# Kernel optimization log

Hardware: AMD Instinct MI355X
Metric: run time of the kernel (lower is better)

Reference implementation:

```python
import jax, jax.numpy as jnp
import numpy as np

B, T, M, D, L = 8, 4096, 32768, 128, 3  # L = ebm_GNN_layer_num - 1


def _lin(x, W, b):
    return x @ W + b


def setup_inputs() -> dict:
    key = jax.random.key(0)
    ks = jax.random.split(key, 24)
    s = 0.05
    inp = {
        "x_1st": jax.random.normal(ks[0], (B, T, 2, D), dtype=jnp.float32),
        "x_2nd": jax.random.normal(ks[1], (B, M, 4, D), dtype=jnp.float32),
        "A_causal": jax.random.uniform(ks[2], (B, 1, M), dtype=jnp.float32),
        "edge": jax.random.randint(ks[3], (2, M), 0, T, dtype=jnp.int64),
        # per-layer node/edge weights (stacked over L layers)
        "node_W": jax.random.normal(ks[4], (L, D, D)) * s,
        "node_b": jnp.zeros((L, D)),
        "mlp_W": jax.random.normal(ks[5], (L, D, D)) * s,
        "mlp_b": jnp.zeros((L, D)),
        "edgeL_W": jax.random.normal(ks[6], (L, D, D)) * s,
        "edgeL_b": jnp.zeros((L, D)),
        # node readout MLP: D -> 2D -> D -> 1
        "nro_W1": jax.random.normal(ks[7], (D, 2 * D)) * s, "nro_b1": jnp.zeros((2 * D,)),
        "nro_W2": jax.random.normal(ks[8], (2 * D, D)) * s, "nro_b2": jnp.zeros((D,)),
        "nro_W3": jax.random.normal(ks[9], (D, 1)) * s, "nro_b3": jnp.zeros((1,)),
        # edge readout MLP
        "ero_W1": jax.random.normal(ks[10], (D, 2 * D)) * s, "ero_b1": jnp.zeros((2 * D,)),
        "ero_W2": jax.random.normal(ks[11], (2 * D, D)) * s, "ero_b2": jnp.zeros((D,)),
        "ero_W3": jax.random.normal(ks[12], (D, 1)) * s, "ero_b3": jnp.zeros((1,)),
    }
    return inp


def reference(x_1st, x_2nd, A_causal, node_W, node_b, mlp_W, mlp_b,
              edgeL_W, edgeL_b, nro_W1, nro_b1, nro_W2, nro_b2, nro_W3, nro_b3,
              ero_W1, ero_b1, ero_W2, ero_b2, ero_W3, ero_b3, edge):
    ni = jnp.array([0, 0, 1, 1])  # node_i_indice
    nj = jnp.array([0, 1, 0, 1])  # node_j_indice
    e0, e1 = edge[0], edge[1]
    a = A_causal[:, 0, :, None, None]  # (B, M, 1, 1)
    xn, xe = x_1st, x_2nd
    for i in range(L):
        # --- node layer: gather -> mask-multiply -> scatter_add -> linear ---
        msg = xn[:, e1] * a                          # (B, M, 2, D)
        upd = jnp.zeros_like(xn).at[:, e0].add(msg)  # (B, T, 2, D)
        xn_new = _lin(xn + upd, node_W[i], node_b[i])
        # --- edge layer (uses updated node features, as in torch forward) ---
        ei = xn_new[:, e0][:, :, ni]                 # (B, M, 4, D)
        ej = xn_new[:, e1][:, :, nj]                 # (B, M, 4, D)
        xe_new = _lin(xe + _lin(ei + ej, mlp_W[i], mlp_b[i]), edgeL_W[i], edgeL_b[i])
        if i < L - 1:
            xn_new = jax.nn.relu(xn_new)
            xe_new = jax.nn.relu(xe_new)
        xn, xe = xn_new, xe_new
    # readouts (dropout=0, concat=False)
    h_node = _lin(jax.nn.relu(_lin(jax.nn.relu(_lin(xn, nro_W1, nro_b1)), nro_W2, nro_b2)), nro_W3, nro_b3)[..., 0]
    h_edge = _lin(jax.nn.relu(_lin(jax.nn.relu(_lin(xe, ero_W1, ero_b1)), ero_W2, ero_b2)), ero_W3, ero_b3)[..., 0]
    return h_node, h_edge  # (B,T,2), (B,M,4)
```

## Files before the change

### kernel.cpp

```cpp
#include <hip/hip_runtime.h>

#define NB 8
#define NT 4096
#define NM 32768
#define ND 128

typedef __attribute__((ext_vector_type(8))) short bf16x8;
typedef __attribute__((ext_vector_type(4))) float f32x4;
typedef __attribute__((ext_vector_type(4))) unsigned int u32x4;

#define MFMA(a,b,c) __builtin_amdgcn_mfma_f32_16x16x32_bf16(a,b,c,0,0,0)

__device__ __forceinline__ unsigned short f2bf(float x) {
  unsigned u = __float_as_uint(x);
  u += 0x7FFFu + ((u >> 16) & 1u);
  return (unsigned short)(u >> 16);
}
__device__ __forceinline__ float bf2f(unsigned short h) {
  return __uint_as_float(((unsigned)h) << 16);
}

__device__ __forceinline__ bf16x8 ldsFrag(const char* lds, int row, int kByte, int rowStride) {
  return *(const bf16x8*)(lds + ((row * rowStride + kByte) ^ ((row & 7) << 4)));
}

__global__ __launch_bounds__(256) void k_prep(
    const float* __restrict__ W, char* __restrict__ dst,
    int K, int N, int khShift, int perShift, int total)
{
  int i = blockIdx.x * 256 + threadIdx.x;
  if (i >= total) return;
  int m  = i >> perShift;
  int j  = i & ((1 << perShift) - 1);
  int n  = j >> khShift;
  int kh = j & ((1 << khShift) - 1);
  int k0 = kh << 3;
  const float* Wm = W + (size_t)m * K * N;
  char* dm = dst + (size_t)m * K * N * 2;
  unsigned short tmp[8];
  #pragma unroll
  for (int jj = 0; jj < 8; ++jj) tmp[jj] = f2bf(Wm[(k0 + jj) * N + n]);
  *(u32x4*)(dm + ((n * K * 2 + k0 * 2) ^ ((n & 7) << 4))) = *(u32x4*)tmp;
}

__global__ __launch_bounds__(256) void k_csr_count(const int* __restrict__ edge, int* deg) {
  int m = blockIdx.x * 256 + threadIdx.x;
  if (m < NM) atomicAdd(&deg[edge[m]], 1);
}
__global__ __launch_bounds__(64) void k_csr_scan(const int* __restrict__ deg,
                                                 int* __restrict__ off, int* __restrict__ cursor) {
  __shared__ int partial[64];
  int t = threadIdx.x;
  int base = t * 64;
  int sum = 0;
  for (int i = 0; i < 64; ++i) sum += deg[base + i];
  partial[t] = sum;
  __syncthreads();
  if (t == 0) {
    int run = 0;
    for (int i = 0; i < 64; ++i) { int v = partial[i]; partial[i] = run; run += v; }
  }
  __syncthreads();
  int run = partial[t];
  for (int i = 0; i < 64; ++i) {
    off[base + i] = run; cursor[base + i] = run;
    run += deg[base + i];
  }
  if (t == 63) off[NT] = NM;
}
__global__ __launch_bounds__(256) void k_csr_fill(const int* __restrict__ edge,
                                                  int* cursor, int* __restrict__ csr) {
  int m = blockIdx.x * 256 + threadIdx.x;
  if (m < NM) { int pos = atomicAdd(&cursor[edge[m]], 1); csr[pos] = m; }
}
__global__ __launch_bounds__(256) void k_csr_sort(const int* __restrict__ off, int* __restrict__ csr) {
  int n = blockIdx.x * 256 + threadIdx.x;
  if (n < NT) {
    int s = off[n], e = off[n + 1];
    for (int i = s + 1; i < e; ++i) {
      int v = csr[i]; int j = i - 1;
      while (j >= s && csr[j] > v) { csr[j + 1] = csr[j]; --j; }
      csr[j + 1] = v;
    }
  }
}

__global__ __launch_bounds__(256, 4) void k_node(
    const float* __restrict__ xnIn, float* __restrict__ xnOut,
    const float* __restrict__ A, const int* __restrict__ edge,
    const int* __restrict__ off, const int* __restrict__ csr,
    const char* __restrict__ WImg, const float* __restrict__ bias,
    int doReluIn, int nTiles)
{
  __shared__ __align__(16) char WT[128 * 256];
  __shared__ __align__(16) char xs[32 * 256];
  const int t = threadIdx.x;
  {
    const u32x4* s = (const u32x4*)WImg;
    u32x4* d = (u32x4*)WT;
    for (int i = t; i < 2048; i += 256) d[i] = s[i];
  }
  const int w   = t >> 6;
  const int l   = t & 63;
  const int l15 = l & 15;
  const int lg  = l >> 4;
  float bv2[2];
  #pragma unroll
  for (int fc = 0; fc < 2; ++fc) bv2[fc] = bias[w * 32 + fc * 16 + l15];
  const int gr = t >> 3;
  const int c0 = (t & 7) << 4;
  __syncthreads();

  for (int tile = blockIdx.x; tile < nTiles; tile += gridDim.x) {
    const int rowBase = tile << 5;
    {
      const int grow = rowBase + gr;
      const int ch   = grow & 1;
      const int node = (grow >> 1) & (NT - 1);
      const int b    = grow >> 13;
      f32x4 acc[4];
      {
        const float4* xr = (const float4*)(xnIn + (size_t)grow * ND + c0);
        #pragma unroll
        for (int q = 0; q < 4; ++q) {
          float4 v = xr[q];
          if (doReluIn) {
            v.x = fmaxf(v.x, 0.f); v.y = fmaxf(v.y, 0.f);
            v.z = fmaxf(v.z, 0.f); v.w = fmaxf(v.w, 0.f);
          }
          acc[q] = (f32x4){v.x, v.y, v.z, v.w};
        }
      }
      const int s = off[node], e = off[node + 1];
      for (int p = s; p < e; ++p) {
        int m = csr[p];
        float a = A[b * NM + m];
        int e1 = edge[NM + m];
        const float4* src = (const float4*)(xnIn + (size_t)(((b * NT + e1) << 1) + ch) * ND + c0);
        #pragma unroll
        for (int q = 0; q < 4; ++q) {
          float4 v = src[q];
          if (doReluIn) {
            v.x = fmaxf(v.x, 0.f); v.y = fmaxf(v.y, 0.f);
            v.z = fmaxf(v.z, 0.f); v.w = fmaxf(v.w, 0.f);
          }
          acc[q][0] = fmaf(a, v.x, acc[q][0]);
          acc[q][1] = fmaf(a, v.y, acc[q][1]);
          acc[q][2] = fmaf(a, v.z, acc[q][2]);
          acc[q][3] = fmaf(a, v.w, acc[q][3]);
        }
      }
      unsigned short tmp[8];
      #pragma unroll
      for (int q = 0; q < 2; ++q)
        #pragma unroll
        for (int j = 0; j < 4; ++j) tmp[q * 4 + j] = f2bf(acc[q][j]);
      *(u32x4*)(xs + ((gr * 256 + c0 * 2) ^ ((gr & 7) << 4))) = *(u32x4*)tmp;
      #pragma unroll
      for (int q = 0; q < 2; ++q)
        #pragma unroll
        for (int j = 0; j < 4; ++j) tmp[q * 4 + j] = f2bf(acc[2 + q][j]);
      *(u32x4*)(xs + ((gr * 256 + c0 * 2 + 16) ^ ((gr & 7) << 4))) = *(u32x4*)tmp;
    }
    __syncthreads();
    f32x4 acc2[2][2];
    #pragma unroll
    for (int fr = 0; fr < 2; ++fr)
      #pragma unroll
      for (int fc = 0; fc < 2; ++fc) acc2[fr][fc] = (f32x4){0.f, 0.f, 0.f, 0.f};
    #pragma unroll
    for (int ks = 0; ks < 4; ++ks) {
      int kb = ks * 64 + lg * 16;
      bf16x8 b0 = ldsFrag(WT, w * 32 + l15,      kb, 256);
      bf16x8 b1 = ldsFrag(WT, w * 32 + 16 + l15, kb, 256);
      bf16x8 a0 = ldsFrag(xs, l15,      kb, 256);
      bf16x8 a1 = ldsFrag(xs, 16 + l15, kb, 256);
      acc2[0][0] = MFMA(a0, b0, acc2[0][0]);
      acc2[0][1] = MFMA(a0, b1, acc2[0][1]);
      acc2[1][0] = MFMA(a1, b0, acc2[1][0]);
      acc2[1][1] = MFMA(a1, b1, acc2[1][1]);
    }
    __syncthreads();
    #pragma unroll
    for (int fr = 0; fr < 2; ++fr)
      #pragma unroll
      for (int fc = 0; fc < 2; ++fc) {
        int col = w * 32 + fc * 16 + l15;
        #pragma unroll
        for (int i = 0; i < 4; ++i) {
          int r = fr * 16 + lg * 4 + i;
          xnOut[(size_t)(rowBase + r) * ND + col] = acc2[fr][fc][i] + bv2[fc];
        }
      }
  }
}

template<int IN_F32>
__global__ __launch_bounds__(512, 4) void k_edge_mfma(
    const float* __restrict__ xn,
    const float* __restrict__ xeInF, const unsigned short* __restrict__ xeInH,
    unsigned short* xeOut,
    const int* __restrict__ edge,
    const char* __restrict__ WmImg, const float* __restrict__ bm,
    const char* __restrict__ WeImg, const float* __restrict__ be,
    int doReluOut, int nTiles)
{
  __shared__ __align__(16) char WmT[128 * 256];
  __shared__ __align__(16) char WeT[128 * 256];
  __shared__ __align__(16) char sA[64 * 256];
  const int t = threadIdx.x;
  {
    const u32x4* sm = (const u32x4*)WmImg;
    const u32x4* se = (const u32x4*)WeImg;
    u32x4* dm = (u32x4*)WmT;
    u32x4* de = (u32x4*)WeT;
    for (int i = t; i < 2048; i += 512) { dm[i] = sm[i]; de[i] = se[i]; }
  }
  const int w   = t >> 6;
  const int l   = t & 63;
  const int l15 = l & 15;
  const int lg  = l >> 4;
  const int rg2 = w >> 2;
  const int wc  = w & 3;
  float bmv[2], bev[2];
  #pragma unroll
  for (int fc = 0; fc < 2; ++fc) {
    int col = wc * 32 + fc * 16 + l15;
    bmv[fc] = bm[col];
    bev[fc] = be[col];
  }
  const int srow = t >> 3;
  __syncthreads();

  for (int tile = blockIdx.x; tile < nTiles; tile += gridDim.x) {
    const int rowBase = tile << 6;
    {
      int grow = rowBase + srow;
      int cch = grow & 3;
      int m = (grow >> 2) & (NM - 1);
      int b = grow >> 17;
      int e0 = edge[m], e1 = edge[NM + m];
      const float4* p0 = (const float4*)(xn + (size_t)((b * NT + e0) * 2 + (cch >> 1)) * ND);
      const float4* p1 = (const float4*)(xn + (size_t)((b * NT + e1) * 2 + (cch & 1)) * ND);
      #pragma unroll
      for (int hh = 0; hh < 2; ++hh) {
        int h = (t & 7) + hh * 8;
        float4 a0 = p0[h * 2], a1 = p0[h * 2 + 1];
        float4 c0 = p1[h * 2], c1 = p1[h * 2 + 1];
        unsigned short tmp[8];
        tmp[0] = f2bf(a0.x + c0.x); tmp[1] = f2bf(a0.y + c0.y);
        tmp[2] = f2bf(a0.z + c0.z); tmp[3] = f2bf(a0.w + c0.w);
        tmp[4] = f2bf(a1.x + c1.x); tmp[5] = f2bf(a1.y + c1.y);
        tmp[6] = f2bf(a1.z + c1.z); tmp[7] = f2bf(a1.w + c1.w);
        *(u32x4*)(sA + ((srow * 256 + h * 16) ^ ((srow & 7) << 4))) = *(u32x4*)tmp;
      }
    }
    float xev[2][2][4];
    #pragma unroll
    for (int fr = 0; fr < 2; ++fr)
      #pragma unroll
      for (int fc = 0; fc < 2; ++fc) {
        int col = wc * 32 + fc * 16 + l15;
        #pragma unroll
        for (int i = 0; i < 4; ++i) {
          int r = rg2 * 32 + fr * 16 + lg * 4 + i;
          size_t idx = (size_t)(rowBase + r) * ND + col;
          xev[fr][fc][i] = IN_F32 ? xeInF[idx] : bf2f(xeInH[idx]);
        }
      }
    __syncthreads();
    f32x4 acc[2][2];
    #pragma unroll
    for (int fr = 0; fr < 2; ++fr)
      #pragma unroll
      for (int fc = 0; fc < 2; ++fc) acc[fr][fc] = (f32x4){0.f, 0.f, 0.f, 0.f};
    #pragma unroll
    for (int ks = 0; ks < 4; ++ks) {
      int kb = ks * 64 + lg * 16;
      bf16x8 b0 = ldsFrag(WmT, wc * 32 + l15,      kb, 256);
      bf16x8 b1 = ldsFrag(WmT, wc * 32 + 16 + l15, kb, 256);
      #pragma unroll
      for (int fr = 0; fr < 2; ++fr) {
        bf16x8 a = ldsFrag(sA, rg2 * 32 + fr * 16 + l15, kb, 256);
        acc[fr][0] = MFMA(a, b0, acc[fr][0]);
        acc[fr][1] = MFMA(a, b1, acc[fr][1]);
      }
    }
    __syncthreads();
    #pragma unroll
    for (int fr = 0; fr < 2; ++fr)
      #pragma unroll
      for (int fc = 0; fc < 2; ++fc) {
        int col = wc * 32 + fc * 16 + l15;
        #pragma unroll
        for (int i = 0; i < 4; ++i) {
          int r = rg2 * 32 + fr * 16 + lg * 4 + i;
          float v = xev[fr][fc][i] + acc[fr][fc][i] + bmv[fc];
          *(unsigned short*)(sA + ((r * 256 + col * 2) ^ ((r & 7) << 4))) = f2bf(v);
        }
      }
    __syncthreads();
    #pragma unroll
    for (int fr = 0; fr < 2; ++fr)
      #pragma unroll
      for (int fc = 0; fc < 2; ++fc) acc[fr][fc] = (f32x4){0.f, 0.f, 0.f, 0.f};
    #pragma unroll
    for (int ks = 0; ks < 4; ++ks) {
      int kb = ks * 64 + lg * 16;
      bf16x8 b0 = ldsFrag(WeT, wc * 32 + l15,      kb, 256);
      bf16x8 b1 = ldsFrag(WeT, wc * 32 + 16 + l15, kb, 256);
      #pragma unroll
      for (int fr = 0; fr < 2; ++fr) {
        bf16x8 a = ldsFrag(sA, rg2 * 32 + fr * 16 + l15, kb, 256);
        acc[fr][0] = MFMA(a, b0, acc[fr][0]);
        acc[fr][1] = MFMA(a, b1, acc[fr][1]);
      }
    }
    __syncthreads();
    #pragma unroll
    for (int fr = 0; fr < 2; ++fr)
      #pragma unroll
      for (int fc = 0; fc < 2; ++fc) {
        int col = wc * 32 + fc * 16 + l15;
        #pragma unroll
        for (int i = 0; i < 4; ++i) {
          int r = rg2 * 32 + fr * 16 + lg * 4 + i;
          float o = acc[fr][fc][i] + bev[fc];
          if (doReluOut) o = fmaxf(o, 0.f);
          xeOut[(size_t)(rowBase + r) * ND + col] = f2bf(o);
        }
      }
  }
}

template<int INBF16>
__global__ __launch_bounds__(512, 4) void k_ro_fused(
    const float* __restrict__ inF, const unsigned short* __restrict__ inH,
    float* __restrict__ out, int nTiles,
    const char* __restrict__ W1Img, const float* __restrict__ b1,
    const char* __restrict__ W2Img, const float* __restrict__ b2,
    const float* __restrict__ W3, const float* __restrict__ b3)
{
  __shared__ __align__(16) char sA[32 * 256];
  __shared__ __align__(16) char h1[32 * 512];
  __shared__ float red[2][32][8];
  const int t = threadIdx.x;
  const int w   = t >> 6;
  const int l   = t & 63;
  const int l15 = l & 15;
  const int lg  = l >> 4;
  bf16x8 w1f[4][2];
  #pragma unroll
  for (int ks = 0; ks < 4; ++ks)
    #pragma unroll
    for (int fc = 0; fc < 2; ++fc) {
      int n = w * 32 + fc * 16 + l15;
      int kb = ks * 64 + lg * 16;
      w1f[ks][fc] = *(const bf16x8*)(W1Img + ((n * 256 + kb) ^ ((n & 7) << 4)));
    }
  bf16x8 w2f[8];
  #pragma unroll
  for (int ks = 0; ks < 8; ++ks) {
    int n = w * 16 + l15;
    int kb = ks * 64 + lg * 16;
    w2f[ks] = *(const bf16x8*)(W2Img + ((n * 512 + kb) ^ ((n & 7) << 4)));
  }
  float b1v[2];
  #pragma unroll
  for (int fc = 0; fc < 2; ++fc) b1v[fc] = b1[w * 32 + fc * 16 + l15];
  const float b2v = b2[w * 16 + l15];
  const float w3v = W3[w * 16 + l15];
  const float b3v = b3[0];
  const int srow = t >> 4;
  float4 pv0, pv1;
  u32x4 pvH;
  int tile = blockIdx.x;
  if (tile < nTiles) {
    if (INBF16) {
      pvH = *(const u32x4*)((const char*)inH + (size_t)((tile << 5) + srow) * 256 + (t & 15) * 16);
    } else {
      const float4* p = (const float4*)(inF + (size_t)((tile << 5) + srow) * ND + (t & 15) * 8);
      pv0 = p[0]; pv1 = p[1];
    }
  }

  int par = 0;
  int prevRow = -1;
  for (; tile < nTiles; tile += gridDim.x) {
    const int rowBase = tile << 5;
    {
      u32x4 vv;
      if (INBF16) {
        vv = pvH;
      } else {
        unsigned short tmp[8];
        tmp[0] = f2bf(pv0.x); tmp[1] = f2bf(pv0.y); tmp[2] = f2bf(pv0.z); tmp[3] = f2bf(pv0.w);
        tmp[4] = f2bf(pv1.x); tmp[5] = f2bf(pv1.y); tmp[6] = f2bf(pv1.z); tmp[7] = f2bf(pv1.w);
        vv = *(u32x4*)tmp;
      }
      *(u32x4*)(sA + ((srow * 256 + (t & 15) * 16) ^ ((srow & 7) << 4))) = vv;
    }
    __syncthreads();
    if (prevRow >= 0 && t < 32) {
      float s = b3v;
      #pragma unroll
      for (int q = 0; q < 8; ++q) s += red[par ^ 1][t][q];
      out[prevRow + t] = s;
    }
    {
      int nt2 = tile + (int)gridDim.x;
      if (nt2 < nTiles) {
        if (INBF16) {
          pvH = *(const u32x4*)((const char*)inH + (size_t)((nt2 << 5) + srow) * 256 + (t & 15) * 16);
        } else {
          const float4* p = (const float4*)(inF + (size_t)((nt2 << 5) + srow) * ND + (t & 15) * 8);
          pv0 = p[0]; pv1 = p[1];
        }
      }
    }
    {
      f32x4 acc[2][2];
      #pragma unroll
      for (int fr = 0; fr < 2; ++fr)
        #pragma unroll
        for (int fc = 0; fc < 2; ++fc) acc[fr][fc] = (f32x4){0.f, 0.f, 0.f, 0.f};
      #pragma unroll
      for (int ks = 0; ks < 4; ++ks) {
        int kb = ks * 64 + lg * 16;
        bf16x8 a0 = ldsFrag(sA, l15,      kb, 256);
        bf16x8 a1 = ldsFrag(sA, 16 + l15, kb, 256);
        acc[0][0] = MFMA(a0, w1f[ks][0], acc[0][0]);
        acc[0][1] = MFMA(a0, w1f[ks][1], acc[0][1]);
        acc[1][0] = MFMA(a1, w1f[ks][0], acc[1][0]);
        acc[1][1] = MFMA(a1, w1f[ks][1], acc[1][1]);
      }
      __syncthreads();
      #pragma unroll
      for (int fr = 0; fr < 2; ++fr)
        #pragma unroll
        for (int fc = 0; fc < 2; ++fc) {
          int col = w * 32 + fc * 16 + l15;
          #pragma unroll
          for (int i = 0; i < 4; ++i) {
            int r = fr * 16 + lg * 4 + i;
            float o = fmaxf(acc[fr][fc][i] + b1v[fc], 0.f);
            *(unsigned short*)(h1 + ((r * 512 + col * 2) ^ ((r & 7) << 4))) = f2bf(o);
          }
        }
    }
    __syncthreads();
    {
      f32x4 acc[2];
      acc[0] = (f32x4){0.f, 0.f, 0.f, 0.f};
      acc[1] = (f32x4){0.f, 0.f, 0.f, 0.f};
      #pragma unroll
      for (int ks = 0; ks < 8; ++ks) {
        int kb = ks * 64 + lg * 16;
        bf16x8 a0 = ldsFrag(h1, l15,      kb, 512);
        bf16x8 a1 = ldsFrag(h1, 16 + l15, kb, 512);
        acc[0] = MFMA(a0, w2f[ks], acc[0]);
        acc[1] = MFMA(a1, w2f[ks], acc[1]);
      }
      #pragma unroll
      for (int fr = 0; fr < 2; ++fr)
        #pragma unroll
        for (int i = 0; i < 4; ++i) {
          float p = fmaxf(acc[fr][i] + b2v, 0.f) * w3v;
          p += __shfl_xor(p, 1);
          p += __shfl_xor(p, 2);
          p += __shfl_xor(p, 4);
          p += __shfl_xor(p, 8);
          if (l15 == 0) red[par][fr * 16 + lg * 4 + i][w] = p;
        }
    }
    prevRow = rowBase;
    par ^= 1;
  }
  __syncthreads();
  if (prevRow >= 0 && t < 32) {
    float s = b3v;
    #pragma unroll
    for (int q = 0; q < 8; ++q) s += red[par ^ 1][t][q];
    out[prevRow + t] = s;
  }
}

extern "C" void kernel_launch(void* const* d_in, const int* in_sizes, int n_in,
                              void* d_out, int out_size, void* d_ws, size_t ws_size,
                              hipStream_t stream)
{
  const float* x1     = (const float*)d_in[0];
  const float* x2     = (const float*)d_in[1];
  const float* Ac     = (const float*)d_in[2];
  const int*   edge   = (const int*)d_in[3];
  const float* node_W = (const float*)d_in[4];
  const float* node_b = (const float*)d_in[5];
  const float* mlp_W  = (const float*)d_in[6];
  const float* mlp_b  = (const float*)d_in[7];
  const float* egL_W  = (const float*)d_in[8];
  const float* egL_b  = (const float*)d_in[9];
  const float* nro_W1 = (const float*)d_in[10];
  const float* nro_b1 = (const float*)d_in[11];
  const float* nro_W2 = (const float*)d_in[12];
  const float* nro_b2 = (const float*)d_in[13];
  const float* nro_W3 = (const float*)d_in[14];
  const float* nro_b3 = (const float*)d_in[15];
  const float* ero_W1 = (const float*)d_in[16];
  const float* ero_b1 = (const float*)d_in[17];
  const float* ero_W2 = (const float*)d_in[18];
  const float* ero_b2 = (const float*)d_in[19];
  const float* ero_W3 = (const float*)d_in[20];
  const float* ero_b3 = (const float*)d_in[21];
  float* out = (float*)d_out;

  const size_t xnElems = (size_t)NB * NT * 2 * ND;
  const size_t xeElems = (size_t)NB * NM * 4 * ND;
  const size_t wBytes  = 3 * 128 * 128 * 2 * 3
                       + 4 * (128 * 256 * 2);
  if (ws_size < xnElems * 2 * sizeof(float) + xeElems * 2 + wBytes) return;

  float* xnA = (float*)d_ws;
  float* xnB = xnA + xnElems;
  unsigned short* xeH = (unsigned short*)(xnB + xnElems);
  char*  wWm = (char*)(xeH + xeElems);
  char*  wWe = wWm + 3 * 128 * 128 * 2;
  char*  wNd = wWe + 3 * 128 * 128 * 2;
  char*  wN1 = wNd + 3 * 128 * 128 * 2;
  char*  wN2 = wN1 + 128 * 256 * 2;
  char*  wE1 = wN2 + 128 * 256 * 2;
  char*  wE2 = wE1 + 128 * 256 * 2;

  int* deg    = (int*)d_out;
  int* off    = deg + NT;
  int* cursor = off + NT + 1;
  int* csr    = cursor + NT;

  k_prep<<<24, 256, 0, stream>>>(mlp_W, wWm, 128, 128, 4, 11, 3 * 2048);
  k_prep<<<24, 256, 0, stream>>>(egL_W, wWe, 128, 128, 4, 11, 3 * 2048);
  k_prep<<<24, 256, 0, stream>>>(node_W, wNd, 128, 128, 4, 11, 3 * 2048);
  k_prep<<<16, 256, 0, stream>>>(nro_W1, wN1, 128, 256, 4, 12, 4096);
  k_prep<<<16, 256, 0, stream>>>(nro_W2, wN2, 256, 128, 5, 12, 4096);
  k_prep<<<16, 256, 0, stream>>>(ero_W1, wE1, 128, 256, 4, 12, 4096);
  k_prep<<<16, 256, 0, stream>>>(ero_W2, wE2, 256, 128, 5, 12, 4096);

  hipMemsetAsync(deg, 0, NT * sizeof(int), stream);
  k_csr_count<<<NM / 256, 256, 0, stream>>>(edge, deg);
  k_csr_scan<<<1, 64, 0, stream>>>(deg, off, cursor);
  k_csr_fill<<<NM / 256, 256, 0, stream>>>(edge, cursor, csr);
  k_csr_sort<<<NT / 256, 256, 0, stream>>>(off, csr);

  const int eTiles = (NB * NM * 4) / 64;
  const int nTilesN = (NB * NT * 2) / 32;
  k_node<<<1024, 256, 0, stream>>>(x1, xnA, Ac, edge, off, csr, wNd, node_b, 0, nTilesN);
  k_edge_mfma<1><<<512, 512, 0, stream>>>(xnA, x2, nullptr, xeH, edge,
                                          wWm, mlp_b, wWe, egL_b, 1, eTiles);
  k_node<<<1024, 256, 0, stream>>>(xnA, xnB, Ac, edge, off, csr,
                                   wNd + 128 * 128 * 2, node_b + ND, 1, nTilesN);
  k_edge_mfma<0><<<512, 512, 0, stream>>>(xnB, nullptr, xeH, xeH, edge,
                                          wWm + 128 * 128 * 2, mlp_b + ND,
                                          wWe + 128 * 128 * 2, egL_b + ND, 1, eTiles);
  k_node<<<1024, 256, 0, stream>>>(xnB, xnA, Ac, edge, off, csr,
                                   wNd + 2 * 128 * 128 * 2, node_b + 2 * ND, 1, nTilesN);
  k_edge_mfma<0><<<512, 512, 0, stream>>>(xnA, nullptr, xeH, xeH, edge,
                                          wWm + 2 * 128 * 128 * 2, mlp_b + 2 * ND,
                                          wWe + 2 * 128 * 128 * 2, egL_b + 2 * ND, 0, eTiles);
  k_ro_fused<0><<<1024, 512, 0, stream>>>(xnA, nullptr, out, (NB * NT * 2) / 32,
                                          wN1, nro_b1, wN2, nro_b2, nro_W3, nro_b3);
  k_ro_fused<1><<<1024, 512, 0, stream>>>(nullptr, xeH, out + NB * NT * 2, (NB * NM * 4) / 32,
                                          wE1, ero_b1, wE2, ero_b2, ero_W3, ero_b3);
}
```

Measured before the change: 1.290 ms.

## Double readout kernel row tile to 64 and drop redundant barrier

The fused readout MLP kernel now processes 64 rows per tile instead of 32, loading twice as much input per thread and running four MFMA row fragments against the register-resident weights. One __syncthreads between the first GEMM and the h1 write is removed, since the top-of-loop barrier already orders it. The grid is reduced to 768 blocks. Larger LDS buffers lower occupancy, while register pressure from more accumulators rises in exchange for better weight reuse and fewer barriers per row.

```diff
diff --git a/kernel.cpp b/kernel.cpp
--- a/kernel.cpp
+++ b/kernel.cpp
@@ -341,9 +341,9 @@
     const char* __restrict__ W2Img, const float* __restrict__ b2,
     const float* __restrict__ W3, const float* __restrict__ b3)
 {
-  __shared__ __align__(16) char sA[32 * 256];
-  __shared__ __align__(16) char h1[32 * 512];
-  __shared__ float red[2][32][8];
+  __shared__ __align__(16) char sA[64 * 256];
+  __shared__ __align__(16) char h1[64 * 512];
+  __shared__ float red[2][64][8];
   const int t = threadIdx.x;
   const int w   = t >> 6;
   const int l   = t & 63;
@@ -371,37 +371,44 @@
   const float b2v = b2[w * 16 + l15];
   const float w3v = W3[w * 16 + l15];
   const float b3v = b3[0];
-  const int srow = t >> 4;
-  float4 pv0, pv1;
-  u32x4 pvH;
+  const int srow  = t >> 3;
+  const int sbyte = (t & 7) << 5;
+  float4 pv[4];
+  u32x4 pvH[2];
   int tile = blockIdx.x;
   if (tile < nTiles) {
     if (INBF16) {
-      pvH = *(const u32x4*)((const char*)inH + (size_t)((tile << 5) + srow) * 256 + (t & 15) * 16);
+      const char* p = (const char*)inH + (size_t)((tile << 6) + srow) * 256 + sbyte;
+      pvH[0] = *(const u32x4*)p;
+      pvH[1] = *(const u32x4*)(p + 16);
     } else {
-      const float4* p = (const float4*)(inF + (size_t)((tile << 5) + srow) * ND + (t & 15) * 8);
-      pv0 = p[0]; pv1 = p[1];
+      const float4* p = (const float4*)(inF + (size_t)((tile << 6) + srow) * ND + (sbyte >> 1));
+      pv[0] = p[0]; pv[1] = p[1]; pv[2] = p[2]; pv[3] = p[3];
     }
   }
 
   int par = 0;
   int prevRow = -1;
   for (; tile < nTiles; tile += gridDim.x) {
-    const int rowBase = tile << 5;
+    const int rowBase = tile << 6;
     {
-      u32x4 vv;
+      u32x4 v0, v1;
       if (INBF16) {
-        vv = pvH;
+        v0 = pvH[0]; v1 = pvH[1];
       } else {
-        unsigned short tmp[8];
-        tmp[0] = f2bf(pv0.x); tmp[1] = f2bf(pv0.y); tmp[2] = f2bf(pv0.z); tmp[3] = f2bf(pv0.w);
-        tmp[4] = f2bf(pv1.x); tmp[5] = f2bf(pv1.y); tmp[6] = f2bf(pv1.z); tmp[7] = f2bf(pv1.w);
-        vv = *(u32x4*)tmp;
-      }
-      *(u32x4*)(sA + ((srow * 256 + (t & 15) * 16) ^ ((srow & 7) << 4))) = vv;
-    }
-    __syncthreads();
-    if (prevRow >= 0 && t < 32) {
+        unsigned short tmp[16];
+        #pragma unroll
+        for (int q = 0; q < 4; ++q) {
+          tmp[q * 4 + 0] = f2bf(pv[q].x); tmp[q * 4 + 1] = f2bf(pv[q].y);
+          tmp[q * 4 + 2] = f2bf(pv[q].z); tmp[q * 4 + 3] = f2bf(pv[q].w);
+        }
+        v0 = *(u32x4*)tmp; v1 = *(u32x4*)(tmp + 8);
+      }
+      *(u32x4*)(sA + ((srow * 256 + sbyte) ^ ((srow & 7) << 4))) = v0;
+      *(u32x4*)(sA + ((srow * 256 + sbyte + 16) ^ ((srow & 7) << 4))) = v1;
+    }
+    __syncthreads();
+    if (prevRow >= 0 && t < 64) {
       float s = b3v;
       #pragma unroll
       for (int q = 0; q < 8; ++q) s += red[par ^ 1][t][q];
@@ -411,32 +418,33 @@
       int nt2 = tile + (int)gridDim.x;
       if (nt2 < nTiles) {
         if (INBF16) {
-          pvH = *(const u32x4*)((const char*)inH + (size_t)((nt2 << 5) + srow) * 256 + (t & 15) * 16);
+          const char* p = (const char*)inH + (size_t)((nt2 << 6) + srow) * 256 + sbyte;
+          pvH[0] = *(const u32x4*)p;
+          pvH[1] = *(const u32x4*)(p + 16);
         } else {
-          const float4* p = (const float4*)(inF + (size_t)((nt2 << 5) + srow) * ND + (t & 15) * 8);
-          pv0 = p[0]; pv1 = p[1];
+          const float4* p = (const float4*)(inF + (size_t)((nt2 << 6) + srow) * ND + (sbyte >> 1));
+          pv[0] = p[0]; pv[1] = p[1]; pv[2] = p[2]; pv[3] = p[3];
         }
       }
     }
     {
-      f32x4 acc[2][2];
-      #pragma unroll
-      for (int fr = 0; fr < 2; ++fr)
+      f32x4 acc[4][2];
+      #pragma unroll
+      for (int fr = 0; fr < 4; ++fr)
         #pragma unroll
         for (int fc = 0; fc < 2; ++fc) acc[fr][fc] = (f32x4){0.f, 0.f, 0.f, 0.f};
       #pragma unroll
       for (int ks = 0; ks < 4; ++ks) {
         int kb = ks * 64 + lg * 16;
-        bf16x8 a0 = ldsFrag(sA, l15,      kb, 256);
-        bf16x8 a1 = ldsFrag(sA, 16 + l15, kb, 256);
-        acc[0][0] = MFMA(a0, w1f[ks][0], acc[0][0]);
-        acc[0][1] = MFMA(a0, w1f[ks][1], acc[0][1]);
-        acc[1][0] = MFMA(a1, w1f[ks][0], acc[1][0]);
-        acc[1][1] = MFMA(a1, w1f[ks][1], acc[1][1]);
-      }
-      __syncthreads();
-      #pragma unroll
-      for (int fr = 0; fr < 2; ++fr)
+        #pragma unroll
+        for (int fr = 0; fr < 4; ++fr) {
+          bf16x8 a = ldsFrag(sA, fr * 16 + l15, kb, 256);
+          acc[fr][0] = MFMA(a, w1f[ks][0], acc[fr][0]);
+          acc[fr][1] = MFMA(a, w1f[ks][1], acc[fr][1]);
+        }
+      }
+      #pragma unroll
+      for (int fr = 0; fr < 4; ++fr)
         #pragma unroll
         for (int fc = 0; fc < 2; ++fc) {
           int col = w * 32 + fc * 16 + l15;
@@ -450,19 +458,20 @@
     }
     __syncthreads();
     {
-      f32x4 acc[2];
-      acc[0] = (f32x4){0.f, 0.f, 0.f, 0.f};
-      acc[1] = (f32x4){0.f, 0.f, 0.f, 0.f};
+      f32x4 acc[4];
+      #pragma unroll
+      for (int fr = 0; fr < 4; ++fr) acc[fr] = (f32x4){0.f, 0.f, 0.f, 0.f};
       #pragma unroll
       for (int ks = 0; ks < 8; ++ks) {
         int kb = ks * 64 + lg * 16;
-        bf16x8 a0 = ldsFrag(h1, l15,      kb, 512);
-        bf16x8 a1 = ldsFrag(h1, 16 + l15, kb, 512);
-        acc[0] = MFMA(a0, w2f[ks], acc[0]);
-        acc[1] = MFMA(a1, w2f[ks], acc[1]);
-      }
-      #pragma unroll
-      for (int fr = 0; fr < 2; ++fr)
+        #pragma unroll
+        for (int fr = 0; fr < 4; ++fr) {
+          bf16x8 a = ldsFrag(h1, fr * 16 + l15, kb, 512);
+          acc[fr] = MFMA(a, w2f[ks], acc[fr]);
+        }
+      }
+      #pragma unroll
+      for (int fr = 0; fr < 4; ++fr)
         #pragma unroll
         for (int i = 0; i < 4; ++i) {
           float p = fmaxf(acc[fr][i] + b2v, 0.f) * w3v;
@@ -477,7 +486,7 @@
     par ^= 1;
   }
   __syncthreads();
-  if (prevRow >= 0 && t < 32) {
+  if (prevRow >= 0 && t < 64) {
     float s = b3v;
     #pragma unroll
     for (int q = 0; q < 8; ++q) s += red[par ^ 1][t][q];
@@ -564,8 +573,8 @@
   k_edge_mfma<0><<<512, 512, 0, stream>>>(xnA, nullptr, xeH, xeH, edge,
                                           wWm + 2 * 128 * 128 * 2, mlp_b + 2 * ND,
                                           wWe + 2 * 128 * 128 * 2, egL_b + 2 * ND, 0, eTiles);
-  k_ro_fused<0><<<1024, 512, 0, stream>>>(xnA, nullptr, out, (NB * NT * 2) / 32,
-                                          wN1, nro_b1, wN2, nro_b2, nro_W3, nro_b3);
-  k_ro_fused<1><<<1024, 512, 0, stream>>>(nullptr, xeH, out + NB * NT * 2, (NB * NM * 4) / 32,
-                                          wE1, ero_b1, wE2, ero_b2, ero_W3, ero_b3);
-}
+  k_ro_fused<0><<<768, 512, 0, stream>>>(xnA, nullptr, out, (NB * NT * 2) / 64,
+                                         wN1, nro_b1, wN2, nro_b2, nro_W3, nro_b3);
+  k_ro_fused<1><<<768, 512, 0, stream>>>(nullptr, xeH, out + NB * NT * 2, (NB * NM * 4) / 64,
+                                         wE1, ero_b1, wE2, ero_b2, ero_W3, ero_b3);
+}
```

New measurement: 2.176 ms. 1.69x slower.

## Hold edge-kernel weight fragments in registers and double-buffer the LDS A tile

Applied to the files above, without the earlier changes.

The edge MFMA kernel no longer stages both 32KB weight matrices in shared memory. Each lane loads its B fragments for both GEMMs straight from the pre-swizzled global image into registers once. A second LDS buffer sB takes the intermediate so two barriers per tile can be dropped, and the grid is doubled to 1024 blocks because LDS use falls from 80KB to 32KB per block. This raises occupancy and removes LDS reads of the weights, at the cost of 64 extra VGPRs per thread, which could cause spilling under launch_bounds(512,4).

```diff
diff --git a/kernel.cpp b/kernel.cpp
--- a/kernel.cpp
+++ b/kernel.cpp
@@ -205,23 +205,25 @@
     const char* __restrict__ WeImg, const float* __restrict__ be,
     int doReluOut, int nTiles)
 {
-  __shared__ __align__(16) char WmT[128 * 256];
-  __shared__ __align__(16) char WeT[128 * 256];
   __shared__ __align__(16) char sA[64 * 256];
+  __shared__ __align__(16) char sB[64 * 256];
   const int t = threadIdx.x;
-  {
-    const u32x4* sm = (const u32x4*)WmImg;
-    const u32x4* se = (const u32x4*)WeImg;
-    u32x4* dm = (u32x4*)WmT;
-    u32x4* de = (u32x4*)WeT;
-    for (int i = t; i < 2048; i += 512) { dm[i] = sm[i]; de[i] = se[i]; }
-  }
   const int w   = t >> 6;
   const int l   = t & 63;
   const int l15 = l & 15;
   const int lg  = l >> 4;
   const int rg2 = w >> 2;
   const int wc  = w & 3;
+  bf16x8 wmf[4][2], wef[4][2];
+  #pragma unroll
+  for (int ks = 0; ks < 4; ++ks)
+    #pragma unroll
+    for (int fc = 0; fc < 2; ++fc) {
+      int n = wc * 32 + fc * 16 + l15;
+      int kb = ks * 64 + lg * 16;
+      wmf[ks][fc] = *(const bf16x8*)(WmImg + ((n * 256 + kb) ^ ((n & 7) << 4)));
+      wef[ks][fc] = *(const bf16x8*)(WeImg + ((n * 256 + kb) ^ ((n & 7) << 4)));
+    }
   float bmv[2], bev[2];
   #pragma unroll
   for (int fc = 0; fc < 2; ++fc) {
@@ -230,7 +232,6 @@
     bev[fc] = be[col];
   }
   const int srow = t >> 3;
-  __syncthreads();
 
   for (int tile = blockIdx.x; tile < nTiles; tile += gridDim.x) {
     const int rowBase = tile << 6;
@@ -277,16 +278,13 @@
     #pragma unroll
     for (int ks = 0; ks < 4; ++ks) {
       int kb = ks * 64 + lg * 16;
-      bf16x8 b0 = ldsFrag(WmT, wc * 32 + l15,      kb, 256);
-      bf16x8 b1 = ldsFrag(WmT, wc * 32 + 16 + l15, kb, 256);
       #pragma unroll
       for (int fr = 0; fr < 2; ++fr) {
         bf16x8 a = ldsFrag(sA, rg2 * 32 + fr * 16 + l15, kb, 256);
-        acc[fr][0] = MFMA(a, b0, acc[fr][0]);
-        acc[fr][1] = MFMA(a, b1, acc[fr][1]);
-      }
-    }
-    __syncthreads();
+        acc[fr][0] = MFMA(a, wmf[ks][0], acc[fr][0]);
+        acc[fr][1] = MFMA(a, wmf[ks][1], acc[fr][1]);
+      }
+    }
     #pragma unroll
     for (int fr = 0; fr < 2; ++fr)
       #pragma unroll
@@ -296,7 +294,7 @@
         for (int i = 0; i < 4; ++i) {
           int r = rg2 * 32 + fr * 16 + lg * 4 + i;
           float v = xev[fr][fc][i] + acc[fr][fc][i] + bmv[fc];
-          *(unsigned short*)(sA + ((r * 256 + col * 2) ^ ((r & 7) << 4))) = f2bf(v);
+          *(unsigned short*)(sB + ((r * 256 + col * 2) ^ ((r & 7) << 4))) = f2bf(v);
         }
       }
     __syncthreads();
@@ -307,16 +305,13 @@
     #pragma unroll
     for (int ks = 0; ks < 4; ++ks) {
       int kb = ks * 64 + lg * 16;
-      bf16x8 b0 = ldsFrag(WeT, wc * 32 + l15,      kb, 256);
-      bf16x8 b1 = ldsFrag(WeT, wc * 32 + 16 + l15, kb, 256);
       #pragma unroll
       for (int fr = 0; fr < 2; ++fr) {
-        bf16x8 a = ldsFrag(sA, rg2 * 32 + fr * 16 + l15, kb, 256);
-        acc[fr][0] = MFMA(a, b0, acc[fr][0]);
-        acc[fr][1] = MFMA(a, b1, acc[fr][1]);
-      }
-    }
-    __syncthreads();
+        bf16x8 a = ldsFrag(sB, rg2 * 32 + fr * 16 + l15, kb, 256);
+        acc[fr][0] = MFMA(a, wef[ks][0], acc[fr][0]);
+        acc[fr][1] = MFMA(a, wef[ks][1], acc[fr][1]);
+      }
+    }
     #pragma unroll
     for (int fr = 0; fr < 2; ++fr)
       #pragma unroll
@@ -552,18 +547,18 @@
   const int eTiles = (NB * NM * 4) / 64;
   const int nTilesN = (NB * NT * 2) / 32;
   k_node<<<1024, 256, 0, stream>>>(x1, xnA, Ac, edge, off, csr, wNd, node_b, 0, nTilesN);
-  k_edge_mfma<1><<<512, 512, 0, stream>>>(xnA, x2, nullptr, xeH, edge,
-                                          wWm, mlp_b, wWe, egL_b, 1, eTiles);
+  k_edge_mfma<1><<<1024, 512, 0, stream>>>(xnA, x2, nullptr, xeH, edge,
+                                           wWm, mlp_b, wWe, egL_b, 1, eTiles);
   k_node<<<1024, 256, 0, stream>>>(xnA, xnB, Ac, edge, off, csr,
                                    wNd + 128 * 128 * 2, node_b + ND, 1, nTilesN);
-  k_edge_mfma<0><<<512, 512, 0, stream>>>(xnB, nullptr, xeH, xeH, edge,
-                                          wWm + 128 * 128 * 2, mlp_b + ND,
-                                          wWe + 128 * 128 * 2, egL_b + ND, 1, eTiles);
+  k_edge_mfma<0><<<1024, 512, 0, stream>>>(xnB, nullptr, xeH, xeH, edge,
+                                           wWm + 128 * 128 * 2, mlp_b + ND,
+                                           wWe + 128 * 128 * 2, egL_b + ND, 1, eTiles);
   k_node<<<1024, 256, 0, stream>>>(xnB, xnA, Ac, edge, off, csr,
                                    wNd + 2 * 128 * 128 * 2, node_b + 2 * ND, 1, nTilesN);
-  k_edge_mfma<0><<<512, 512, 0, stream>>>(xnA, nullptr, xeH, xeH, edge,
-                                          wWm + 2 * 128 * 128 * 2, mlp_b + 2 * ND,
-                                          wWe + 2 * 128 * 128 * 2, egL_b + 2 * ND, 0, eTiles);
+  k_edge_mfma<0><<<1024, 512, 0, stream>>>(xnA, nullptr, xeH, xeH, edge,
+                                           wWm + 2 * 128 * 128 * 2, mlp_b + 2 * ND,
+                                           wWe + 2 * 128 * 128 * 2, egL_b + 2 * ND, 0, eTiles);
   k_ro_fused<0><<<1024, 512, 0, stream>>>(xnA, nullptr, out, (NB * NT * 2) / 32,
                                           wN1, nro_b1, wN2, nro_b2, nro_W3, nro_b3);
   k_ro_fused<1><<<1024, 512, 0, stream>>>(nullptr, xeH, out + NB * NT * 2, (NB * NM * 4) / 32,
```

Result: slower. 2.258 ms (+75.0%).
